# Performance work log

Hardware: AMD Instinct MI355X
Metric: run time of the kernel (lower is better)

The kernel has to match this reference:

```python
import jax, jax.numpy as jnp
import numpy as np

B, T, H, P, N = 32, 512, 128, 16, 16
D = 4 * H


def _lstm(x, Wih, Whh, bih, bhh):
    # standard torch-style LSTM, batch_first input x: [B, T, 1], zero init state
    Bz = x.shape[0]
    Hh = Whh.shape[1]
    h0 = jnp.zeros((Bz, Hh), x.dtype)

    def step(carry, xt):
        h, c = carry
        g = xt @ Wih.T + bih + h @ Whh.T + bhh  # [B, 4H], gate order i,f,g,o
        i, f, gg, o = jnp.split(g, 4, axis=-1)
        c = jax.nn.sigmoid(f) * c + jax.nn.sigmoid(i) * jnp.tanh(gg)
        h = jax.nn.sigmoid(o) * jnp.tanh(c)
        return (h, c), h

    _, hs = jax.lax.scan(step, (h0, h0), jnp.swapaxes(x, 0, 1))
    return jnp.swapaxes(hs, 0, 1)  # [B, T, H]


def _forward(Y, Xp, Xn, Xi, init_c, init_h, Wih, Whh, bih, bhh,
             Wc, Uc, bc, Wg, Ug, bg, Wf, Uf, bf, Wo, Uo, bo, Wa,
             Watt, batt, vatt, W1, b1, W2, b2, W3, b3):
    run = lambda x: _lstm(x, Wih, Whh, bih, bhh)
    Y1 = run(Y)                                              # [B,T,H]
    Xi1 = run(Xi)
    Xp1 = jnp.mean(jax.vmap(run)(jnp.moveaxis(Xp, 1, 0)), axis=0)  # mean over P stocks
    Xn1 = jnp.mean(jax.vmap(run)(jnp.moveaxis(Xn, 1, 0)), axis=0)
    result = jnp.concatenate([Y1, Xp1, Xn1, Xi1], axis=2)    # [B,T,4H]

    Hh = Wa.shape[0]

    def mi_step(carry, xt):  # Mi-LSTM cell: 4 input streams with gated-candidate attention
        c, h = carry
        xs = xt.reshape(xt.shape[0], 4, Hh)                  # split 4H into 4 streams
        cand = jnp.tanh(jnp.einsum('bkh,khj->bkj', xs, Wc) + jnp.einsum('bh,khj->bkj', h, Uc) + bc)
        ig = jax.nn.sigmoid(jnp.einsum('bkh,khj->bkj', xs, Wg) + jnp.einsum('bh,khj->bkj', h, Ug) + bg)
        l = ig * cand                                        # [B,4,H]
        a = jax.nn.softmax(jnp.einsum('bkj,bj->bk', l, c @ Wa), axis=1)
        lmix = jnp.einsum('bk,bkj->bj', a, l)
        f = jax.nn.sigmoid(xt @ Wf + h @ Uf + bf)
        o = jax.nn.sigmoid(xt @ Wo + h @ Uo + bo)
        c = f * c + lmix
        h = o * jnp.tanh(c)
        return (c, h), h

    _, hs = jax.lax.scan(mi_step, (init_c, init_h), jnp.swapaxes(result, 0, 1))
    Y2 = jnp.swapaxes(hs, 0, 1)                              # [B,T,H]

    # temporal attention over the Mi-LSTM outputs
    scores = jnp.tanh(Y2 @ Watt + batt) @ vatt               # [B,T]
    attw = jax.nn.softmax(scores, axis=1)
    Y3 = jnp.einsum('bt,bth->bh', attw, Y2)                  # [B,H]

    hm = jax.nn.relu(Y3 @ W1 + b1)
    hm = jax.nn.relu(hm @ W2 + b2)
    return hm @ W3 + b3                                      # [B,1]


def setup_inputs() -> dict:
    key = jax.random.key(0)
    ks = jax.random.split(key, 24)
    u = lambda k, s: jax.random.uniform(k, s, dtype=jnp.float32)
    nr = lambda k, s: jax.random.normal(k, s, dtype=jnp.float32) * 0.05
    z = lambda s: jnp.zeros(s, jnp.float32)
    return {
        'Y': u(ks[0], (B, T, 1)), 'Xp': u(ks[1], (B, P, T, 1)), 'Xn': u(ks[2], (B, N, T, 1)),
        'Xi': u(ks[3], (B, T, 1)), 'Target': u(ks[4], (B, 1)),
        'init_c': u(ks[5], (B, H)), 'init_h': u(ks[6], (B, H)),
        'Wih': nr(ks[7], (4 * H, 1)), 'Whh': nr(ks[8], (4 * H, H)), 'bih': z(4 * H), 'bhh': z(4 * H),
        'Wc': nr(ks[9], (4, H, H)), 'Uc': nr(ks[10], (4, H, H)), 'bc': z((4, H)),
        'Wg': nr(ks[11], (4, H, H)), 'Ug': nr(ks[12], (4, H, H)), 'bg': z((4, H)),
        'Wf': nr(ks[13], (D, H)), 'Uf': nr(ks[14], (H, H)), 'bf': z(H),
        'Wo': nr(ks[15], (D, H)), 'Uo': nr(ks[16], (H, H)), 'bo': z(H),
        'Wa': nr(ks[17], (H, H)),
        'Watt': nr(ks[18], (H, H)), 'batt': z(H), 'vatt': nr(ks[19], (H,)),
        'W1': nr(ks[20], (H, H)), 'b1': z(H),
        'W2': nr(ks[21], (H, H)), 'b2': z(H),
        'W3': nr(ks[22], (H, 1)), 'b3': z(1),
    }


def reference(Y, Xp, Xn, Xi, Target, init_c, init_h, Wih, Whh, bih, bhh,
              Wc, Uc, bc, Wg, Ug, bg, Wf, Uf, bf, Wo, Uo, bo, Wa,
              Watt, batt, vatt, W1, b1, W2, b2, W3, b3):
    out = _forward(Y, Xp, Xn, Xi, init_c, init_h, Wih, Whh, bih, bhh,
                   Wc, Uc, bc, Wg, Ug, bg, Wf, Uf, bf, Wo, Uo, bo, Wa,
                   Watt, batt, vatt, W1, b1, W2, b2, W3, b3)
    loss = jnp.mean((out - Target) ** 2)
    return out, loss
```

## Files before the change

kernel.cpp:

```cpp
#include <hip/hip_runtime.h>
#include <hip/hip_fp16.h>

typedef _Float16 half8 __attribute__((ext_vector_type(8)));
typedef float float4_ __attribute__((ext_vector_type(4)));

__device__ __forceinline__ float rcp_(float x) { return __builtin_amdgcn_rcpf(x); }
__device__ __forceinline__ float sigf(float x) { return rcp_(1.f + __expf(-x)); }
__device__ __forceinline__ float tanhf2(float x) {
  x = fminf(fmaxf(x, -15.f), 15.f);
  float e = __expf(-2.f * x);
  return (1.f - e) * rcp_(1.f + e);
}

#define DOT2F16(acc, w, h) asm("v_dot2_f32_f16 %0, %1, %2, %0" : "+v"(acc) : "v"(w), "v"(h))

__global__ __launch_bounds__(512, 2)
void k1_lstm(const float* __restrict__ Y, const float* __restrict__ Xp,
             const float* __restrict__ Xn, const float* __restrict__ Xi,
             const float* __restrict__ Wih, const float* __restrict__ Whh,
             const float* __restrict__ bih, const float* __restrict__ bhh,
             _Float16* __restrict__ result)
{
  __shared__ float x_lds[16][513];
  __shared__ _Float16 hbuf[2][16][136];

  const int tid  = threadIdx.x;
  const int wv   = tid >> 6;
  const int lane = tid & 63;
  const int cl   = lane & 15;
  const int rowg = lane >> 4;
  const int bid  = blockIdx.x;

  const float* xsrc; int slot; int do_mean; int b_out_base;
  if (bid < 2)       { xsrc = Y  + (size_t)(bid * 16) * 512;        slot = 0; do_mean = 0; b_out_base = bid * 16; }
  else if (bid < 4)  { xsrc = Xi + (size_t)((bid - 2) * 16) * 512;  slot = 3; do_mean = 0; b_out_base = (bid - 2) * 16; }
  else if (bid < 36) { xsrc = Xp + (size_t)((bid - 4) * 16) * 512;  slot = 1; do_mean = 1; b_out_base = bid - 4; }
  else               { xsrc = Xn + (size_t)((bid - 36) * 16) * 512; slot = 2; do_mean = 1; b_out_base = bid - 36; }

  for (int i = tid; i < 16 * 512; i += 512) {
    int r = i >> 9, t = i & 511;
    x_lds[r][t] = xsrc[r * 512 + t];
  }
  for (int i = tid; i < 16 * 136; i += 512) {
    hbuf[0][i / 136][i % 136] = (_Float16)0.f;
  }

  const int cg = wv * 16 + cl;
  half8 bw[4][4];
  #pragma unroll
  for (int g = 0; g < 4; ++g) {
    #pragma unroll
    for (int kc = 0; kc < 4; ++kc) {
      const float* p = Whh + (size_t)(g * 128 + cg) * 128 + kc * 32 + rowg * 8;
      half8 v;
      #pragma unroll
      for (int j = 0; j < 8; ++j) v[j] = (_Float16)p[j];
      bw[g][kc] = v;
    }
  }
  float wih_r[4], bias_r[4];
  #pragma unroll
  for (int g = 0; g < 4; ++g) {
    wih_r[g]  = Wih[g * 128 + cg];
    bias_r[g] = bih[g * 128 + cg] + bhh[g * 128 + cg];
  }

  float c_reg[4] = {0.f, 0.f, 0.f, 0.f};
  __syncthreads();

  for (int t = 0; t < 512; ++t) {
    const int cur = t & 1;
    half8 a[4];
    #pragma unroll
    for (int kc = 0; kc < 4; ++kc)
      a[kc] = *(const half8*)&hbuf[cur][cl][kc * 32 + rowg * 8];

    float4_ acc[4];
    #pragma unroll
    for (int g = 0; g < 4; ++g) {
      float4_ z = {0.f, 0.f, 0.f, 0.f};
      #pragma unroll
      for (int kc = 0; kc < 4; ++kc)
        z = __builtin_amdgcn_mfma_f32_16x16x32_f16(a[kc], bw[g][kc], z, 0, 0, 0);
      acc[g] = z;
    }

    float hv[4];
    #pragma unroll
    for (int i = 0; i < 4; ++i) {
      const int row = rowg * 4 + i;
      float x  = x_lds[row][t];
      float ui = acc[0][i] + x * wih_r[0] + bias_r[0];
      float uf = acc[1][i] + x * wih_r[1] + bias_r[1];
      float ug = acc[2][i] + x * wih_r[2] + bias_r[2];
      float uo = acc[3][i] + x * wih_r[3] + bias_r[3];
      float ii = sigf(ui), ff = sigf(uf), gg = tanhf2(ug), oo = sigf(uo);
      float c  = ff * c_reg[i] + ii * gg;
      c_reg[i] = c;
      float h  = oo * tanhf2(c);
      hv[i] = h;
      hbuf[cur ^ 1][row][cg] = (_Float16)h;
    }

    if (!do_mean) {
      #pragma unroll
      for (int i = 0; i < 4; ++i) {
        int b = b_out_base + rowg * 4 + i;
        result[(((size_t)b * 512 + t) * 4 + slot) * 128 + cg] = (_Float16)hv[i];
      }
    } else {
      float s = hv[0] + hv[1] + hv[2] + hv[3];
      s += __shfl_xor(s, 16, 64);
      s += __shfl_xor(s, 32, 64);
      if (rowg == 0)
        result[(((size_t)b_out_base * 512 + t) * 4 + slot) * 128 + cg] = (_Float16)(s * 0.0625f);
    }
    __syncthreads();
  }
}

__global__ __launch_bounds__(512, 2)
void k2_gemm(const _Float16* __restrict__ result,
             const float* __restrict__ Wc, const float* __restrict__ Wg,
             const float* __restrict__ Wf, const float* __restrict__ Wo,
             _Float16* __restrict__ candX, _Float16* __restrict__ igX,
             _Float16* __restrict__ fX, _Float16* __restrict__ oX)
{
  __shared__ _Float16 a_lds[128][136];
  __shared__ _Float16 bt_lds[256][136];

  const int tid   = threadIdx.x;
  const int lane  = tid & 63;
  const int wv    = tid >> 6;
  const int cl    = lane & 15, rowg = lane >> 4;
  const int mtile = blockIdx.x;
  const int role  = blockIdx.y;

  const int nchunks = (role == 0) ? 4 : 1;
  const int kstream = role - 1;

  float4_ acc[16];
  #pragma unroll
  for (int n = 0; n < 16; ++n) acc[n] = (float4_){0.f, 0.f, 0.f, 0.f};

  for (int ch = 0; ch < nchunks; ++ch) {
    const int koff = (role == 0) ? ch * 128 : kstream * 128;
    for (int i = tid; i < 1024; i += 512) {
      int r = i >> 3, v8 = i & 7;
      half8 val = *(const half8*)&result[((size_t)(mtile * 128 + r)) * 512 + koff + v8 * 8];
      *(half8*)&a_lds[r][v8 * 8] = val;
    }
    for (int i = tid; i < 128 * 256; i += 512) {
      int n = i & 255, kk = i >> 8;
      float w;
      if (role == 0) {
        w = (n < 128) ? Wf[(size_t)(ch * 128 + kk) * 128 + n]
                      : Wo[(size_t)(ch * 128 + kk) * 128 + (n - 128)];
      } else {
        w = (n < 128) ? Wc[(size_t)(kstream * 128 + kk) * 128 + n]
                      : Wg[(size_t)(kstream * 128 + kk) * 128 + (n - 128)];
      }
      bt_lds[n][kk] = (_Float16)w;
    }
    __syncthreads();
    #pragma unroll
    for (int kc = 0; kc < 4; ++kc) {
      half8 a = *(const half8*)&a_lds[wv * 16 + cl][kc * 32 + rowg * 8];
      #pragma unroll
      for (int n = 0; n < 16; ++n) {
        half8 bb = *(const half8*)&bt_lds[n * 16 + cl][kc * 32 + rowg * 8];
        acc[n] = __builtin_amdgcn_mfma_f32_16x16x32_f16(a, bb, acc[n], 0, 0, 0);
      }
    }
    __syncthreads();
  }

  #pragma unroll
  for (int n = 0; n < 16; ++n) {
    int col = n * 16 + cl;
    #pragma unroll
    for (int i = 0; i < 4; ++i) {
      size_t r = (size_t)mtile * 128 + wv * 16 + rowg * 4 + i;
      _Float16 v = (_Float16)acc[n][i];
      if (role == 0) {
        if (col < 128) fX[r * 128 + col] = v;
        else           oX[r * 128 + (col - 128)] = v;
      } else {
        if (col < 128) candX[(r * 4 + kstream) * 128 + col] = v;
        else           igX  [(r * 4 + kstream) * 128 + (col - 128)] = v;
      }
    }
  }
}

#define PRELOAD(arr, sbase)                                                 \
  {                                                                         \
    const int s = tid + sbase;                                              \
    const float* src; float mul = 1.f;                                      \
    if (s < 512)       src = Uc + (s >> 7) * 16384 + (s & 127);             \
    else if (s < 1024) src = Ug + ((s >> 7) - 4) * 16384 + (s & 127);       \
    else if (s < 1152) src = Uf + (s - 1024);                               \
    else if (s < 1280) src = Uo + (s - 1152);                               \
    else if (s < 1408) src = Wa + (s - 1280);                               \
    else             { src = Wa; mul = 0.f; }                               \
    _Pragma("unroll")                                                       \
    for (int d = 0; d < 64; ++d) {                                          \
      union { _Float16 h[2]; unsigned u; } cv;                              \
      cv.h[0] = (_Float16)(src[(2 * d) * 128] * mul);                       \
      cv.h[1] = (_Float16)(src[(2 * d + 1) * 128] * mul);                   \
      arr[d] = cv.u;                                                        \
    }                                                                       \
  }

__global__ __launch_bounds__(512, 2)
void k3_scan(const float* __restrict__ Uc, const float* __restrict__ Ug,
             const float* __restrict__ Uf, const float* __restrict__ Uo,
             const float* __restrict__ Wa,
             const float* __restrict__ bc, const float* __restrict__ bg,
             const float* __restrict__ bfv, const float* __restrict__ bov,
             const float* __restrict__ init_c, const float* __restrict__ init_h,
             const _Float16* __restrict__ candX, const _Float16* __restrict__ igX,
             const _Float16* __restrict__ fX, const _Float16* __restrict__ oX,
             _Float16* __restrict__ Y2)
{
  __shared__ __align__(16) unsigned h_pk[64];
  __shared__ __align__(16) unsigned c_pk[64];
  __shared__ float c_f32[128];
  __shared__ float raw[1536];
  __shared__ float part2[2][4];

  const int tid = threadIdx.x;
  const int b   = blockIdx.x;

  unsigned wpk0[64], wpk1[64], wpk2[64];
  PRELOAD(wpk0, 0)
  PRELOAD(wpk1, 512)
  PRELOAD(wpk2, 1024)

  float bc_r[4] = {0, 0, 0, 0}, bg_r[4] = {0, 0, 0, 0}, bf_r = 0.f, bo_r = 0.f;
  if (tid < 128) {
    #pragma unroll
    for (int k = 0; k < 4; ++k) { bc_r[k] = bc[k * 128 + tid]; bg_r[k] = bg[k * 128 + tid]; }
    bf_r = bfv[tid]; bo_r = bov[tid];
    c_f32[tid] = init_c[b * 128 + tid];
  }
  if (tid < 64) {
    union { _Float16 h[2]; unsigned u; } hp, cp;
    hp.h[0] = (_Float16)init_h[b * 128 + 2 * tid];
    hp.h[1] = (_Float16)init_h[b * 128 + 2 * tid + 1];
    cp.h[0] = (_Float16)init_c[b * 128 + 2 * tid];
    cp.h[1] = (_Float16)init_c[b * 128 + 2 * tid + 1];
    h_pk[tid] = hp.u;
    c_pk[tid] = cp.u;
  }
  __syncthreads();

  const int slot3 = tid + 1024;

  for (int t = 0; t < 512; ++t) {
    float cx[4] = {0, 0, 0, 0}, gx[4] = {0, 0, 0, 0}, fx = 0.f, ox = 0.f;
    if (tid < 128) {
      size_t r = (size_t)b * 512 + t;
      #pragma unroll
      for (int k = 0; k < 4; ++k) {
        cx[k] = (float)candX[(r * 4 + k) * 128 + tid];
        gx[k] = (float)igX  [(r * 4 + k) * 128 + tid];
      }
      fx = (float)fX[r * 128 + tid];
      ox = (float)oX[r * 128 + tid];
    }

    float a1 = 0.f, a2 = 0.f, a3 = 0.f;
    {
      const uint4* hp4 = (const uint4*)h_pk;
      if (tid < 256 || tid >= 384) {
        #pragma unroll
        for (int g = 0; g < 16; ++g) {
          uint4 hv = hp4[g];
          DOT2F16(a1, wpk0[4*g+0], hv.x); DOT2F16(a2, wpk1[4*g+0], hv.x); DOT2F16(a3, wpk2[4*g+0], hv.x);
          DOT2F16(a1, wpk0[4*g+1], hv.y); DOT2F16(a2, wpk1[4*g+1], hv.y); DOT2F16(a3, wpk2[4*g+1], hv.y);
          DOT2F16(a1, wpk0[4*g+2], hv.z); DOT2F16(a2, wpk1[4*g+2], hv.z); DOT2F16(a3, wpk2[4*g+2], hv.z);
          DOT2F16(a1, wpk0[4*g+3], hv.w); DOT2F16(a2, wpk1[4*g+3], hv.w); DOT2F16(a3, wpk2[4*g+3], hv.w);
        }
      } else {
        const uint4* cp4 = (const uint4*)c_pk;
        #pragma unroll
        for (int g = 0; g < 16; ++g) {
          uint4 hv = hp4[g]; uint4 hc = cp4[g];
          DOT2F16(a1, wpk0[4*g+0], hv.x); DOT2F16(a2, wpk1[4*g+0], hv.x); DOT2F16(a3, wpk2[4*g+0], hc.x);
          DOT2F16(a1, wpk0[4*g+1], hv.y); DOT2F16(a2, wpk1[4*g+1], hv.y); DOT2F16(a3, wpk2[4*g+1], hc.y);
          DOT2F16(a1, wpk0[4*g+2], hv.z); DOT2F16(a2, wpk1[4*g+2], hv.z); DOT2F16(a3, wpk2[4*g+2], hc.z);
          DOT2F16(a1, wpk0[4*g+3], hv.w); DOT2F16(a2, wpk1[4*g+3], hv.w); DOT2F16(a3, wpk2[4*g+3], hc.w);
        }
      }
    }
    raw[tid]       = a1;
    raw[tid + 512] = a2;
    raw[slot3]     = a3;
    __syncthreads();

    float l0 = 0.f, l1 = 0.f, l2 = 0.f, l3 = 0.f, fj = 0.f, oj = 0.f;
    if (tid < 128) {
      float cand[4], ig[4];
      #pragma unroll
      for (int k = 0; k < 4; ++k) {
        float uc = cx[k] + raw[k * 128 + tid] + bc_r[k];
        float ui = gx[k] + raw[512 + k * 128 + tid] + bg_r[k];
        cand[k] = tanhf2(uc);
        ig[k]   = sigf(ui);
      }
      l0 = ig[0] * cand[0]; l1 = ig[1] * cand[1];
      l2 = ig[2] * cand[2]; l3 = ig[3] * cand[3];
      float cwa = raw[1280 + tid];
      float p0 = l0 * cwa, p1 = l1 * cwa, p2 = l2 * cwa, p3 = l3 * cwa;
      #pragma unroll
      for (int m = 1; m < 64; m <<= 1) {
        p0 += __shfl_xor(p0, m, 64);
        p1 += __shfl_xor(p1, m, 64);
        p2 += __shfl_xor(p2, m, 64);
        p3 += __shfl_xor(p3, m, 64);
      }
      if ((tid & 63) == 0) {
        part2[tid >> 6][0] = p0; part2[tid >> 6][1] = p1;
        part2[tid >> 6][2] = p2; part2[tid >> 6][3] = p3;
      }
      fj = sigf(fx + raw[1024 + tid] + bf_r);
      oj = sigf(ox + raw[1152 + tid] + bo_r);
    }
    __syncthreads();

    if (tid < 128) {
      float d0 = part2[0][0] + part2[1][0];
      float d1 = part2[0][1] + part2[1][1];
      float d2 = part2[0][2] + part2[1][2];
      float d3 = part2[0][3] + part2[1][3];
      float mx = fmaxf(fmaxf(d0, d1), fmaxf(d2, d3));
      float e0 = __expf(d0 - mx), e1 = __expf(d1 - mx);
      float e2 = __expf(d2 - mx), e3 = __expf(d3 - mx);
      float inv = rcp_(e0 + e1 + e2 + e3);
      float lmix = (e0 * l0 + e1 * l1 + e2 * l2 + e3 * l3) * inv;
      float c = fj * c_f32[tid] + lmix;
      c_f32[tid] = c;
      float h = oj * tanhf2(c);
      ((_Float16*)h_pk)[tid] = (_Float16)h;
      ((_Float16*)c_pk)[tid] = (_Float16)c;
      Y2[((size_t)b * 512 + t) * 128 + tid] = (_Float16)h;
    }
    __syncthreads();
  }
}

__global__ __launch_bounds__(256, 1)
void k4_attn(const _Float16* __restrict__ Y2,
             const float* __restrict__ Watt, const float* __restrict__ batt,
             const float* __restrict__ vatt,
             const float* __restrict__ W1, const float* __restrict__ b1,
             const float* __restrict__ W2, const float* __restrict__ b2,
             const float* __restrict__ W3, const float* __restrict__ b3,
             float* __restrict__ out)
{
  __shared__ _Float16 wt_lds[128][136];
  __shared__ float sc[512];
  __shared__ float red[8];
  __shared__ float y3[128];
  __shared__ float hm[128];

  const int tid = threadIdx.x;
  const int b   = blockIdx.x;
  const int lane = tid & 63, wv = tid >> 6;
  const int cl = lane & 15, rowg = lane >> 4;

  for (int i = tid; i < 128 * 128; i += 256) {
    int h = i >> 7, j = i & 127;
    wt_lds[j][h] = (_Float16)Watt[h * 128 + j];
  }
  __syncthreads();

  half8 bw[8][4];
  #pragma unroll
  for (int n = 0; n < 8; ++n)
    #pragma unroll
    for (int kc = 0; kc < 4; ++kc)
      bw[n][kc] = *(const half8*)&wt_lds[n * 16 + cl][kc * 32 + rowg * 8];
  float battr[8], vattr[8];
  #pragma unroll
  for (int n = 0; n < 8; ++n) { battr[n] = batt[n * 16 + cl]; vattr[n] = vatt[n * 16 + cl]; }

  for (int mt = wv * 8; mt < wv * 8 + 8; ++mt) {
    half8 a[4];
    #pragma unroll
    for (int kc = 0; kc < 4; ++kc)
      a[kc] = *(const half8*)&Y2[((size_t)b * 512 + mt * 16 + cl) * 128 + kc * 32 + rowg * 8];
    float sp[4] = {0.f, 0.f, 0.f, 0.f};
    #pragma unroll
    for (int n = 0; n < 8; ++n) {
      float4_ acc = {0.f, 0.f, 0.f, 0.f};
      #pragma unroll
      for (int kc = 0; kc < 4; ++kc)
        acc = __builtin_amdgcn_mfma_f32_16x16x32_f16(a[kc], bw[n][kc], acc, 0, 0, 0);
      #pragma unroll
      for (int i = 0; i < 4; ++i)
        sp[i] += tanhf2(acc[i] + battr[n]) * vattr[n];
    }
    #pragma unroll
    for (int i = 0; i < 4; ++i) {
      #pragma unroll
      for (int m = 1; m < 16; m <<= 1) sp[i] += __shfl_xor(sp[i], m, 64);
    }
    if (cl == 0) {
      #pragma unroll
      for (int i = 0; i < 4; ++i) sc[mt * 16 + rowg * 4 + i] = sp[i];
    }
  }
  __syncthreads();

  float v0 = sc[tid], v1 = sc[tid + 256];
  float mx = fmaxf(v0, v1);
  #pragma unroll
  for (int m = 1; m < 64; m <<= 1) mx = fmaxf(mx, __shfl_xor(mx, m, 64));
  if (lane == 0) red[wv] = mx;
  __syncthreads();
  mx = fmaxf(fmaxf(red[0], red[1]), fmaxf(red[2], red[3]));
  float e0 = __expf(v0 - mx), e1 = __expf(v1 - mx);
  float s = e0 + e1;
  #pragma unroll
  for (int m = 1; m < 64; m <<= 1) s += __shfl_xor(s, m, 64);
  __syncthreads();
  if (lane == 0) red[wv] = s;
  __syncthreads();
  float inv = rcp_(red[0] + red[1] + red[2] + red[3]);
  sc[tid] = e0 * inv;
  sc[tid + 256] = e1 * inv;
  __syncthreads();

  {
    int h = tid & 127, part = tid >> 7;
    float acc = 0.f;
    for (int t = part * 256; t < part * 256 + 256; ++t)
      acc += sc[t] * (float)Y2[((size_t)b * 512 + t) * 128 + h];
    if (part == 0) y3[h] = acc;
    __syncthreads();
    if (part == 1) y3[h] += acc;
    __syncthreads();
  }

  if (tid < 128) {
    float a1 = 0.f;
    for (int h2 = 0; h2 < 128; ++h2) a1 += y3[h2] * W1[h2 * 128 + tid];
    hm[tid] = fmaxf(a1 + b1[tid], 0.f);
  }
  __syncthreads();
  if (tid < 128) {
    float a2 = 0.f;
    for (int h2 = 0; h2 < 128; ++h2) a2 += hm[h2] * W2[h2 * 128 + tid];
    a2 = fmaxf(a2 + b2[tid], 0.f);
    float p = a2 * W3[tid];
    #pragma unroll
    for (int m = 1; m < 64; m <<= 1) p += __shfl_xor(p, m, 64);
    if ((tid & 63) == 0) red[4 + (tid >> 6)] = p;
  }
  __syncthreads();
  if (tid == 0) out[b] = red[4] + red[5] + b3[0];
}

__global__ void k5_loss(const float* __restrict__ out, const float* __restrict__ target,
                        float* __restrict__ loss_out)
{
  int l = threadIdx.x;
  float v = 0.f;
  if (l < 32) { float d = out[l] - target[l]; v = d * d; }
  #pragma unroll
  for (int m = 1; m < 64; m <<= 1) v += __shfl_xor(v, m, 64);
  if (l == 0) loss_out[0] = v * (1.f / 32.f);
}

extern "C" void kernel_launch(void* const* d_in, const int* in_sizes, int n_in,
                              void* d_out, int out_size, void* d_ws, size_t ws_size,
                              hipStream_t stream)
{
  const float* Y      = (const float*)d_in[0];
  const float* Xp     = (const float*)d_in[1];
  const float* Xn     = (const float*)d_in[2];
  const float* Xi     = (const float*)d_in[3];
  const float* Target = (const float*)d_in[4];
  const float* init_c = (const float*)d_in[5];
  const float* init_h = (const float*)d_in[6];
  const float* Wih    = (const float*)d_in[7];
  const float* Whh    = (const float*)d_in[8];
  const float* bih    = (const float*)d_in[9];
  const float* bhh    = (const float*)d_in[10];
  const float* Wc     = (const float*)d_in[11];
  const float* Uc     = (const float*)d_in[12];
  const float* bc     = (const float*)d_in[13];
  const float* Wg     = (const float*)d_in[14];
  const float* Ug     = (const float*)d_in[15];
  const float* bg     = (const float*)d_in[16];
  const float* Wf     = (const float*)d_in[17];
  const float* Uf     = (const float*)d_in[18];
  const float* bf     = (const float*)d_in[19];
  const float* Wo     = (const float*)d_in[20];
  const float* Uo     = (const float*)d_in[21];
  const float* bo     = (const float*)d_in[22];
  const float* Wa     = (const float*)d_in[23];
  const float* Watt   = (const float*)d_in[24];
  const float* batt   = (const float*)d_in[25];
  const float* vatt   = (const float*)d_in[26];
  const float* W1     = (const float*)d_in[27];
  const float* b1     = (const float*)d_in[28];
  const float* W2     = (const float*)d_in[29];
  const float* b2     = (const float*)d_in[30];
  const float* W3     = (const float*)d_in[31];
  const float* b3     = (const float*)d_in[32];

  char* ws = (char*)d_ws;
  _Float16* result = (_Float16*)(ws);
  _Float16* candX  = (_Float16*)(ws + ((size_t)16 << 20));
  _Float16* igX    = (_Float16*)(ws + ((size_t)32 << 20));
  _Float16* fXp    = (_Float16*)(ws + ((size_t)48 << 20));
  _Float16* oXp    = (_Float16*)(ws + ((size_t)52 << 20));
  _Float16* Y2     = (_Float16*)(ws + ((size_t)56 << 20));
  float* outp = (float*)d_out;

  k1_lstm<<<dim3(68), dim3(512), 0, stream>>>(Y, Xp, Xn, Xi, Wih, Whh, bih, bhh, result);
  k2_gemm<<<dim3(128, 5), dim3(512), 0, stream>>>(result, Wc, Wg, Wf, Wo, candX, igX, fXp, oXp);
  k3_scan<<<dim3(32), dim3(512), 0, stream>>>(Uc, Ug, Uf, Uo, Wa, bc, bg, bf, bo,
                                              init_c, init_h, candX, igX, fXp, oXp, Y2);
  k4_attn<<<dim3(32), dim3(256), 0, stream>>>(Y2, Watt, batt, vatt, W1, b1, W2, b2, W3, b3, outp);
  k5_loss<<<dim3(1), dim3(64), 0, stream>>>(outp, Target, outp + 32);
}
```

Before: 1.667 ms.

## Collapse Mi-LSTM scan epilogue into one wave, drop a barrier, prefetch inputs

The per-step Mi-LSTM epilogue now runs in a single 64-lane wave, with each lane handling two hidden units. This lets the attention-score reduction finish with wave shuffles alone and removes the cross-wave partial buffer and one __syncthreads per timestep. The precomputed input projections for the next step are prefetched into registers, the cell state stays in registers, and the h output store is deferred by one step. The dot-product loops split accumulators for more ILP, and the last wave skips the unused third product. In exchange, the epilogue's transcendental work is serialised onto one wave, which lengthens that phase.

```diff
diff --git a/kernel.cpp b/kernel.cpp
--- a/kernel.cpp
+++ b/kernel.cpp
@@ -10,6 +10,10 @@
   x = fminf(fmaxf(x, -15.f), 15.f);
   float e = __expf(-2.f * x);
   return (1.f - e) * rcp_(1.f + e);
+}
+__device__ __forceinline__ float2 up2(unsigned u) {
+  union { unsigned u; _Float16 h[2]; } cv; cv.u = u;
+  return make_float2((float)cv.h[0], (float)cv.h[1]);
 }
 
 #define DOT2F16(acc, w, h) asm("v_dot2_f32_f16 %0, %1, %2, %0" : "+v"(acc) : "v"(w), "v"(h))
@@ -225,9 +229,7 @@
 {
   __shared__ __align__(16) unsigned h_pk[64];
   __shared__ __align__(16) unsigned c_pk[64];
-  __shared__ float c_f32[128];
-  __shared__ float raw[1536];
-  __shared__ float part2[2][4];
+  __shared__ float raw[1408];
 
   const int tid = threadIdx.x;
   const int b   = blockIdx.x;
@@ -237,117 +239,139 @@
   PRELOAD(wpk1, 512)
   PRELOAD(wpk2, 1024)
 
-  float bc_r[4] = {0, 0, 0, 0}, bg_r[4] = {0, 0, 0, 0}, bf_r = 0.f, bo_r = 0.f;
-  if (tid < 128) {
-    #pragma unroll
-    for (int k = 0; k < 4; ++k) { bc_r[k] = bc[k * 128 + tid]; bg_r[k] = bg[k * 128 + tid]; }
-    bf_r = bfv[tid]; bo_r = bov[tid];
-    c_f32[tid] = init_c[b * 128 + tid];
-  }
+  float c0 = 0.f, c1 = 0.f;
+  float2 bc2[4], bg2[4], bf2 = {0.f, 0.f}, bo2 = {0.f, 0.f};
+  unsigned pf_c[4], pf_g[4], pf_f = 0u, pf_o = 0u;
+  unsigned hprev = 0u;
   if (tid < 64) {
-    union { _Float16 h[2]; unsigned u; } hp, cp;
-    hp.h[0] = (_Float16)init_h[b * 128 + 2 * tid];
-    hp.h[1] = (_Float16)init_h[b * 128 + 2 * tid + 1];
-    cp.h[0] = (_Float16)init_c[b * 128 + 2 * tid];
-    cp.h[1] = (_Float16)init_c[b * 128 + 2 * tid + 1];
-    h_pk[tid] = hp.u;
-    c_pk[tid] = cp.u;
-  }
-  __syncthreads();
-
-  const int slot3 = tid + 1024;
+    float2 ci = *(const float2*)&init_c[b * 128 + 2 * tid];
+    float2 hi = *(const float2*)&init_h[b * 128 + 2 * tid];
+    c0 = ci.x; c1 = ci.y;
+    union { _Float16 h[2]; unsigned u; } hu, cu;
+    hu.h[0] = (_Float16)hi.x; hu.h[1] = (_Float16)hi.y;
+    cu.h[0] = (_Float16)ci.x; cu.h[1] = (_Float16)ci.y;
+    h_pk[tid] = hu.u; c_pk[tid] = cu.u;
+    #pragma unroll
+    for (int k = 0; k < 4; ++k) {
+      bc2[k] = *(const float2*)&bc[k * 128 + 2 * tid];
+      bg2[k] = *(const float2*)&bg[k * 128 + 2 * tid];
+    }
+    bf2 = *(const float2*)&bfv[2 * tid];
+    bo2 = *(const float2*)&bov[2 * tid];
+    size_t r2 = (size_t)b * 512;
+    #pragma unroll
+    for (int k = 0; k < 4; ++k) {
+      pf_c[k] = ((const unsigned*)candX)[r2 * 256 + k * 64 + tid];
+      pf_g[k] = ((const unsigned*)igX)  [r2 * 256 + k * 64 + tid];
+    }
+    pf_f = ((const unsigned*)fX)[r2 * 64 + tid];
+    pf_o = ((const unsigned*)oX)[r2 * 64 + tid];
+  }
+  __syncthreads();
+
+  const uint4* hp4 = (const uint4*)h_pk;
+  const uint4* cp4 = (const uint4*)c_pk;
 
   for (int t = 0; t < 512; ++t) {
-    float cx[4] = {0, 0, 0, 0}, gx[4] = {0, 0, 0, 0}, fx = 0.f, ox = 0.f;
-    if (tid < 128) {
-      size_t r = (size_t)b * 512 + t;
+    if (t > 0 && tid < 64)
+      ((unsigned*)Y2)[((size_t)b * 512 + (t - 1)) * 64 + tid] = hprev;
+
+    float a1a = 0.f, a1b = 0.f, a2a = 0.f, a2b = 0.f, a3a = 0.f, a3b = 0.f;
+    if (tid < 256) {
+      #pragma unroll
+      for (int g = 0; g < 16; ++g) {
+        uint4 hv = hp4[g];
+        DOT2F16(a1a, wpk0[4*g+0], hv.x); DOT2F16(a2a, wpk1[4*g+0], hv.x); DOT2F16(a3a, wpk2[4*g+0], hv.x);
+        DOT2F16(a1b, wpk0[4*g+1], hv.y); DOT2F16(a2b, wpk1[4*g+1], hv.y); DOT2F16(a3b, wpk2[4*g+1], hv.y);
+        DOT2F16(a1a, wpk0[4*g+2], hv.z); DOT2F16(a2a, wpk1[4*g+2], hv.z); DOT2F16(a3a, wpk2[4*g+2], hv.z);
+        DOT2F16(a1b, wpk0[4*g+3], hv.w); DOT2F16(a2b, wpk1[4*g+3], hv.w); DOT2F16(a3b, wpk2[4*g+3], hv.w);
+      }
+    } else if (tid < 384) {
+      #pragma unroll
+      for (int g = 0; g < 16; ++g) {
+        uint4 hv = hp4[g]; uint4 hc = cp4[g];
+        DOT2F16(a1a, wpk0[4*g+0], hv.x); DOT2F16(a2a, wpk1[4*g+0], hv.x); DOT2F16(a3a, wpk2[4*g+0], hc.x);
+        DOT2F16(a1b, wpk0[4*g+1], hv.y); DOT2F16(a2b, wpk1[4*g+1], hv.y); DOT2F16(a3b, wpk2[4*g+1], hc.y);
+        DOT2F16(a1a, wpk0[4*g+2], hv.z); DOT2F16(a2a, wpk1[4*g+2], hv.z); DOT2F16(a3a, wpk2[4*g+2], hc.z);
+        DOT2F16(a1b, wpk0[4*g+3], hv.w); DOT2F16(a2b, wpk1[4*g+3], hv.w); DOT2F16(a3b, wpk2[4*g+3], hc.w);
+      }
+    } else {
+      #pragma unroll
+      for (int g = 0; g < 16; ++g) {
+        uint4 hv = hp4[g];
+        DOT2F16(a1a, wpk0[4*g+0], hv.x); DOT2F16(a2a, wpk1[4*g+0], hv.x);
+        DOT2F16(a1b, wpk0[4*g+1], hv.y); DOT2F16(a2b, wpk1[4*g+1], hv.y);
+        DOT2F16(a1a, wpk0[4*g+2], hv.z); DOT2F16(a2a, wpk1[4*g+2], hv.z);
+        DOT2F16(a1b, wpk0[4*g+3], hv.w); DOT2F16(a2b, wpk1[4*g+3], hv.w);
+      }
+    }
+    raw[tid]       = a1a + a1b;
+    raw[tid + 512] = a2a + a2b;
+    if (tid < 384) raw[1024 + tid] = a3a + a3b;
+    __syncthreads();
+
+    if (tid < 64) {
+      float2 cxv[4], gxv[4];
+      #pragma unroll
+      for (int k = 0; k < 4; ++k) { cxv[k] = up2(pf_c[k]); gxv[k] = up2(pf_g[k]); }
+      float2 fxv = up2(pf_f), oxv = up2(pf_o);
+
+      float2 cwa = *(const float2*)&raw[1280 + 2 * tid];
+      float l0[4], l1[4], p[4];
       #pragma unroll
       for (int k = 0; k < 4; ++k) {
-        cx[k] = (float)candX[(r * 4 + k) * 128 + tid];
-        gx[k] = (float)igX  [(r * 4 + k) * 128 + tid];
-      }
-      fx = (float)fX[r * 128 + tid];
-      ox = (float)oX[r * 128 + tid];
-    }
-
-    float a1 = 0.f, a2 = 0.f, a3 = 0.f;
-    {
-      const uint4* hp4 = (const uint4*)h_pk;
-      if (tid < 256 || tid >= 384) {
+        float2 rc = *(const float2*)&raw[k * 128 + 2 * tid];
+        float2 rg = *(const float2*)&raw[512 + k * 128 + 2 * tid];
+        float ca0 = tanhf2(cxv[k].x + rc.x + bc2[k].x);
+        float ca1 = tanhf2(cxv[k].y + rc.y + bc2[k].y);
+        float g0  = sigf(gxv[k].x + rg.x + bg2[k].x);
+        float g1  = sigf(gxv[k].y + rg.y + bg2[k].y);
+        l0[k] = g0 * ca0; l1[k] = g1 * ca1;
+        p[k]  = l0[k] * cwa.x + l1[k] * cwa.y;
+      }
+      float2 rf = *(const float2*)&raw[1024 + 2 * tid];
+      float2 ro = *(const float2*)&raw[1152 + 2 * tid];
+      float f0 = sigf(fxv.x + rf.x + bf2.x), f1 = sigf(fxv.y + rf.y + bf2.y);
+      float o0 = sigf(oxv.x + ro.x + bo2.x), o1 = sigf(oxv.y + ro.y + bo2.y);
+
+      if (t < 511) {
+        size_t r2 = (size_t)b * 512 + t + 1;
         #pragma unroll
-        for (int g = 0; g < 16; ++g) {
-          uint4 hv = hp4[g];
-          DOT2F16(a1, wpk0[4*g+0], hv.x); DOT2F16(a2, wpk1[4*g+0], hv.x); DOT2F16(a3, wpk2[4*g+0], hv.x);
-          DOT2F16(a1, wpk0[4*g+1], hv.y); DOT2F16(a2, wpk1[4*g+1], hv.y); DOT2F16(a3, wpk2[4*g+1], hv.y);
-          DOT2F16(a1, wpk0[4*g+2], hv.z); DOT2F16(a2, wpk1[4*g+2], hv.z); DOT2F16(a3, wpk2[4*g+2], hv.z);
-          DOT2F16(a1, wpk0[4*g+3], hv.w); DOT2F16(a2, wpk1[4*g+3], hv.w); DOT2F16(a3, wpk2[4*g+3], hv.w);
+        for (int k = 0; k < 4; ++k) {
+          pf_c[k] = ((const unsigned*)candX)[r2 * 256 + k * 64 + tid];
+          pf_g[k] = ((const unsigned*)igX)  [r2 * 256 + k * 64 + tid];
         }
-      } else {
-        const uint4* cp4 = (const uint4*)c_pk;
-        #pragma unroll
-        for (int g = 0; g < 16; ++g) {
-          uint4 hv = hp4[g]; uint4 hc = cp4[g];
-          DOT2F16(a1, wpk0[4*g+0], hv.x); DOT2F16(a2, wpk1[4*g+0], hv.x); DOT2F16(a3, wpk2[4*g+0], hc.x);
-          DOT2F16(a1, wpk0[4*g+1], hv.y); DOT2F16(a2, wpk1[4*g+1], hv.y); DOT2F16(a3, wpk2[4*g+1], hc.y);
-          DOT2F16(a1, wpk0[4*g+2], hv.z); DOT2F16(a2, wpk1[4*g+2], hv.z); DOT2F16(a3, wpk2[4*g+2], hc.z);
-          DOT2F16(a1, wpk0[4*g+3], hv.w); DOT2F16(a2, wpk1[4*g+3], hv.w); DOT2F16(a3, wpk2[4*g+3], hc.w);
-        }
-      }
-    }
-    raw[tid]       = a1;
-    raw[tid + 512] = a2;
-    raw[slot3]     = a3;
-    __syncthreads();
-
-    float l0 = 0.f, l1 = 0.f, l2 = 0.f, l3 = 0.f, fj = 0.f, oj = 0.f;
-    if (tid < 128) {
-      float cand[4], ig[4];
-      #pragma unroll
-      for (int k = 0; k < 4; ++k) {
-        float uc = cx[k] + raw[k * 128 + tid] + bc_r[k];
-        float ui = gx[k] + raw[512 + k * 128 + tid] + bg_r[k];
-        cand[k] = tanhf2(uc);
-        ig[k]   = sigf(ui);
-      }
-      l0 = ig[0] * cand[0]; l1 = ig[1] * cand[1];
-      l2 = ig[2] * cand[2]; l3 = ig[3] * cand[3];
-      float cwa = raw[1280 + tid];
-      float p0 = l0 * cwa, p1 = l1 * cwa, p2 = l2 * cwa, p3 = l3 * cwa;
+        pf_f = ((const unsigned*)fX)[r2 * 64 + tid];
+        pf_o = ((const unsigned*)oX)[r2 * 64 + tid];
+      }
+
       #pragma unroll
       for (int m = 1; m < 64; m <<= 1) {
-        p0 += __shfl_xor(p0, m, 64);
-        p1 += __shfl_xor(p1, m, 64);
-        p2 += __shfl_xor(p2, m, 64);
-        p3 += __shfl_xor(p3, m, 64);
-      }
-      if ((tid & 63) == 0) {
-        part2[tid >> 6][0] = p0; part2[tid >> 6][1] = p1;
-        part2[tid >> 6][2] = p2; part2[tid >> 6][3] = p3;
-      }
-      fj = sigf(fx + raw[1024 + tid] + bf_r);
-      oj = sigf(ox + raw[1152 + tid] + bo_r);
-    }
-    __syncthreads();
-
-    if (tid < 128) {
-      float d0 = part2[0][0] + part2[1][0];
-      float d1 = part2[0][1] + part2[1][1];
-      float d2 = part2[0][2] + part2[1][2];
-      float d3 = part2[0][3] + part2[1][3];
-      float mx = fmaxf(fmaxf(d0, d1), fmaxf(d2, d3));
-      float e0 = __expf(d0 - mx), e1 = __expf(d1 - mx);
-      float e2 = __expf(d2 - mx), e3 = __expf(d3 - mx);
+        p[0] += __shfl_xor(p[0], m, 64);
+        p[1] += __shfl_xor(p[1], m, 64);
+        p[2] += __shfl_xor(p[2], m, 64);
+        p[3] += __shfl_xor(p[3], m, 64);
+      }
+      float mx = fmaxf(fmaxf(p[0], p[1]), fmaxf(p[2], p[3]));
+      float e0 = __expf(p[0] - mx), e1 = __expf(p[1] - mx);
+      float e2 = __expf(p[2] - mx), e3 = __expf(p[3] - mx);
       float inv = rcp_(e0 + e1 + e2 + e3);
-      float lmix = (e0 * l0 + e1 * l1 + e2 * l2 + e3 * l3) * inv;
-      float c = fj * c_f32[tid] + lmix;
-      c_f32[tid] = c;
-      float h = oj * tanhf2(c);
-      ((_Float16*)h_pk)[tid] = (_Float16)h;
-      ((_Float16*)c_pk)[tid] = (_Float16)c;
-      Y2[((size_t)b * 512 + t) * 128 + tid] = (_Float16)h;
-    }
-    __syncthreads();
-  }
+      float lm0 = (e0 * l0[0] + e1 * l0[1] + e2 * l0[2] + e3 * l0[3]) * inv;
+      float lm1 = (e0 * l1[0] + e1 * l1[1] + e2 * l1[2] + e3 * l1[3]) * inv;
+      c0 = f0 * c0 + lm0;
+      c1 = f1 * c1 + lm1;
+      float h0 = o0 * tanhf2(c0), h1 = o1 * tanhf2(c1);
+      union { _Float16 h[2]; unsigned u; } hu, cu;
+      hu.h[0] = (_Float16)h0; hu.h[1] = (_Float16)h1;
+      cu.h[0] = (_Float16)c0; cu.h[1] = (_Float16)c1;
+      h_pk[tid] = hu.u;
+      c_pk[tid] = cu.u;
+      hprev = hu.u;
+    }
+    __syncthreads();
+  }
+  if (tid < 64)
+    ((unsigned*)Y2)[((size_t)b * 512 + 511) * 64 + tid] = hprev;
 }
 
 __global__ __launch_bounds__(256, 1)
```

New measurement: 2.580 ms. +54.7%, slower.
